# Performance work log

Hardware: AMD Instinct MI355X
Metric: run time of the kernel (lower is better)

The kernel has to match this reference:

```python
import jax, jax.numpy as jnp
import numpy as np

CUTOFF = 3.0   # self.cutoff
RMIN = 3.5     # rmin in cutoff_function (note rmin > cutoff, faithful to source)
ETA = 4.0
N_RADIAL = 5
N_3BODY = 12
NATOMS = 2048
K = 48         # neighbors per atom (equal counts -> ragged loop becomes dense batch)
HID = 64
NPAIRS = NATOMS * K


def setup_inputs() -> dict:
    key = jax.random.key(0)
    ks = jax.random.split(key, 4)
    # displacements scaled so |rij| is mostly within a few Angstrom
    rij = jax.random.normal(ks[0], (NPAIRS, 3), jnp.float32) * 1.5
    # sorted-by-atom pair list with K neighbors per atom
    unique_i = jnp.repeat(jnp.arange(NATOMS, dtype=jnp.int64), K)
    W1 = jax.random.normal(ks[1], (N_RADIAL + N_3BODY, HID), jnp.float32) * 0.1
    b1 = jnp.zeros((HID,), jnp.float32)
    W2 = jax.random.normal(ks[2], (HID, HID), jnp.float32) * 0.1
    b2 = jnp.zeros((HID,), jnp.float32)
    W3 = jax.random.normal(ks[3], (HID, 1), jnp.float32) * 0.1
    b3 = jnp.zeros((1,), jnp.float32)
    return dict(rij=rij, unique_i=unique_i, W1=W1, b1=b1, W2=W2, b2=b2, W3=W3, b3=b3)


def _energy(rij, W1, b1, W2, b2, W3, b3):
    d = jnp.linalg.norm(rij, axis=1, keepdims=True)           # (P,1)
    diff_norm = rij / jnp.maximum(d, 1e-12)                   # F.normalize
    # pair cutoff (rmin=3.5, c=3.0 as in source)
    fc = jnp.where(d > RMIN,
                   0.5 + 0.5 * jnp.cos(jnp.pi * (d - RMIN) / (CUTOFF - RMIN)),
                   1.0)
    # radial Bessel basis, n = 1..5
    ns = jnp.arange(1, N_RADIAL + 1, dtype=rij.dtype)
    rbf = jnp.sqrt(2.0 / CUTOFF) * jnp.sin(ns * jnp.pi / CUTOFF * d) / d * fc  # (P,5)
    # 3-body Gaussian descriptors
    fcrik = (0.5 + 0.5 * jnp.cos(jnp.pi * d / CUTOFF))[:, 0]  # (P,)
    dn = diff_norm.reshape(NATOMS, K, 3)
    cosang = jnp.einsum('nkd,nld->nkl', dn, dn)               # (N,K,K) pairwise mm
    cosang = jnp.where(jnp.eye(K, dtype=bool)[None], 0.0, cosang)  # fill_diagonal_(0)
    mu = jnp.linspace(-1.0, 1.0, N_3BODY).astype(rij.dtype)
    w = fcrik.reshape(NATOMS, 1, K, 1)                        # fcrik broadcast on axis being summed
    g3b = jnp.sum(jnp.exp(-ETA * (cosang[..., None] - mu) ** 2) * w, axis=2)  # (N,K,12)
    g3b = g3b.reshape(NPAIRS, N_3BODY)
    desc = jnp.concatenate([rbf, g3b], axis=1)                # (P,17)
    h = jnp.tanh(desc @ W1 + b1)
    h = jnp.tanh(h @ W2 + b2)
    eij = h @ W3 + b3                                         # (P,1)
    return jnp.sum(eij * fc)


def reference(rij, unique_i, W1, b1, W2, b2, W3, b3):
    # Module output: gradients of total energy w.r.t. rij (written into beta)
    return jax.grad(_energy)(rij, W1, b1, W2, b2, W3, b3)
```

## Files before the change

kernel.cpp:

```cpp
#include <hip/hip_runtime.h>
#include <hip/hip_bf16.h>

#define NATOMS 2048
#define K 48
#define P (NATOMS * K)
#define NR 5
#define NM 12
#define ND 17
#define HID 64

#define PI_F 3.14159265358979f
#define CUT 3.0f
#define RMIN_F 3.5f
#define AFC (-6.28318530717959f)
#define POC (PI_F / CUT)
#define SQ 0.816496580927726f
#define E1C 1.45454545454545f
#define CMC (-0.132231404958678f)

__device__ unsigned short g_desc[P * 32];
__device__ float g_gdesc[P * 20];
__device__ unsigned short g_w1t[64 * 32];
__device__ unsigned short g_w2t[64 * 64];
__device__ unsigned short g_w2r[64 * 64];
__device__ unsigned short g_w1r[32 * 64];

using frag_ab = __attribute__((ext_vector_type(8))) short;
using frag_cd = __attribute__((ext_vector_type(4))) float;

__device__ __forceinline__ float fast_tanh(float x) {
    float cx = fminf(fmaxf(x, -15.0f), 15.0f);
    float t = __expf(2.0f * cx);
    return (t - 1.0f) / (t + 1.0f);
}

__device__ __forceinline__ unsigned short f2bs(float x) {
    __hip_bfloat16 b = __float2bfloat16(x);
    return __builtin_bit_cast(unsigned short, b);
}

__global__ __launch_bounds__(256) void k_prep(const float* __restrict__ W1,
                                              const float* __restrict__ W2) {
    const int i = blockIdx.x * 256 + threadIdx.x;
    if (i < 2048) {
        const int n = i >> 5, k = i & 31;
        g_w1t[i] = (k < ND) ? f2bs(W1[k * HID + n]) : (unsigned short)0;
    } else if (i < 2048 + 4096) {
        const int j = i - 2048, n = j >> 6, k = j & 63;
        g_w2t[j] = f2bs(W2[k * HID + n]);
    } else if (i < 2048 + 8192) {
        const int j = i - (2048 + 4096);
        g_w2r[j] = f2bs(W2[j]);
    } else if (i < 2048 + 8192 + 2048) {
        const int j = i - (2048 + 8192), n = j >> 6;
        g_w1r[j] = (n < ND) ? f2bs(W1[j]) : (unsigned short)0;
    }
}

__global__ __launch_bounds__(192) void k_fwd_atom(const float* __restrict__ rij) {
    __shared__ float su[K][3];
    __shared__ float sfcrik[K];
    __shared__ float sc[K * (K + 1)];
    __shared__ float spart[4 * K * 13];
    __shared__ __align__(16) unsigned short sOut[K][32];
    const int atom = blockIdx.x, t = threadIdx.x, base = atom * K;

    if (t < K) {
        const float x = rij[3 * (base + t) + 0];
        const float y = rij[3 * (base + t) + 1];
        const float z = rij[3 * (base + t) + 2];
        const float d = sqrtf(x * x + y * y + z * z);
        const float inv = 1.0f / fmaxf(d, 1e-12f);
        su[t][0] = x * inv; su[t][1] = y * inv; su[t][2] = z * inv;
        sfcrik[t] = 0.5f + 0.5f * __cosf(POC * d);
        const float fc = (d > RMIN_F) ? (0.5f + 0.5f * __cosf(AFC * (d - RMIN_F))) : 1.0f;
        const float s = SQ * fc / d;
#pragma unroll
        for (int n = 0; n < NR; n++) {
            const float bn = (float)(n + 1) * POC;
            sOut[t][n] = f2bs(s * __sinf(bn * d));
        }
#pragma unroll
        for (int c = ND; c < 32; c++) sOut[t][c] = 0;
    }
    __syncthreads();

#pragma unroll
    for (int r = 0; r < 12; r++) {
        const int idx = t + r * 192;
        const int k = idx / K, l = idx - k * K;
        const float c = su[k][0] * su[l][0] + su[k][1] * su[l][1] + su[k][2] * su[l][2];
        sc[k * (K + 1) + l] = (k == l) ? 0.0f : c;
    }
    __syncthreads();

    {
        const int k = t % K, ch = t / K;
        float part[NM];
#pragma unroll
        for (int m = 0; m < NM; m++) part[m] = 0.0f;
#pragma unroll
        for (int li = 0; li < 12; li++) {
            const int l = ch * 12 + li;
            const float cp1 = sc[k * (K + 1) + l] + 1.0f;
            const float e0 = __expf(-4.0f * cp1 * cp1) * sfcrik[l];
            const float e1 = __expf(E1C * cp1);
            float tm = e0;
            part[0] += tm;
#pragma unroll
            for (int m = 1; m < NM; m++) { tm *= e1; part[m] += tm; }
        }
#pragma unroll
        for (int m = 0; m < NM; m++) spart[(ch * K + k) * 13 + m] = part[m];
    }
    __syncthreads();

#pragma unroll
    for (int r = 0; r < 3; r++) {
        const int idx = t + r * 192;
        const int k = idx / NM, m = idx - k * NM;
        const float cm = __expf(CMC * (float)(m * m));
        const float s = spart[(0 * K + k) * 13 + m] + spart[(1 * K + k) * 13 + m]
                      + spart[(2 * K + k) * 13 + m] + spart[(3 * K + k) * 13 + m];
        sOut[k][NR + m] = f2bs(s * cm);
    }
    __syncthreads();

    {
        const int r = t >> 2, c = (t & 3) * 8;
        *(uint4*)&g_desc[(base + r) * 32 + c] = *(const uint4*)&sOut[r][c];
    }
}

#define LW1 40
#define LW2 72
#define O_DESC 0
#define O_W1T  2560
#define O_W2T  5120
#define O_W2R  9728
#define O_W1R  14336
#define O_H1   16640
#define O_GZ2  21248
#define SM_SHORTS 25856

__global__ __launch_bounds__(256) void k_mlp(const float* __restrict__ rij,
                                             const float* __restrict__ b1,
                                             const float* __restrict__ b2,
                                             const float* __restrict__ W3,
                                             const float* __restrict__ b3) {
    __shared__ __align__(16) short sm[SM_SHORTS];
    __shared__ float sFc[64], sB1[64], sB2[64], sW3[64];

    const int t = threadIdx.x;
    const int base = blockIdx.x * 64;

    if (t < 64) {
        const int p = base + t;
        const float x = rij[3 * p], y = rij[3 * p + 1], z = rij[3 * p + 2];
        const float d = sqrtf(x * x + y * y + z * z);
        sFc[t] = (d > RMIN_F) ? (0.5f + 0.5f * __cosf(AFC * (d - RMIN_F))) : 1.0f;
        sB1[t] = b1[t]; sB2[t] = b2[t]; sW3[t] = W3[t];
    }
    {
        const int r = t >> 2, c = (t & 3) * 8;
        *(uint4*)&sm[O_DESC + r * LW1 + c] = *(const uint4*)&g_desc[(base + r) * 32 + c];
    }
    {
        const int n = t >> 2, c = (t & 3) * 8;
        *(uint4*)&sm[O_W1T + n * LW1 + c] = *(const uint4*)&g_w1t[n * 32 + c];
    }
#pragma unroll
    for (int rr = 0; rr < 2; rr++) {
        const int i = t + rr * 256, n = i >> 3, c = (i & 7) * 8;
        *(uint4*)&sm[O_W2T + n * LW2 + c] = *(const uint4*)&g_w2t[n * 64 + c];
    }
#pragma unroll
    for (int rr = 0; rr < 2; rr++) {
        const int i = t + rr * 256, n = i >> 3, c = (i & 7) * 8;
        *(uint4*)&sm[O_W2R + n * LW2 + c] = *(const uint4*)&g_w2r[n * 64 + c];
    }
    {
        const int n = t >> 3, c = (t & 7) * 8;
        *(uint4*)&sm[O_W1R + n * LW2 + c] = *(const uint4*)&g_w1r[n * 64 + c];
    }
    __syncthreads();

    const int w = t >> 6, lane = t & 63, quad = lane >> 4, lm = lane & 15;
    const int mrow = w * 16;

    float t1[16];
    {
        const frag_ab a = *(const frag_ab*)&sm[O_DESC + (mrow + lm) * LW1 + quad * 8];
#pragma unroll
        for (int nt = 0; nt < 4; nt++) {
            const frag_ab bf = *(const frag_ab*)&sm[O_W1T + (nt * 16 + lm) * LW1 + quad * 8];
            const float bias = sB1[nt * 16 + lm];
            frag_cd acc = {bias, bias, bias, bias};
            acc = __builtin_amdgcn_mfma_f32_16x16x32_bf16(a, bf, acc, 0, 0, 0);
#pragma unroll
            for (int r = 0; r < 4; r++) {
                const float tv = fast_tanh(acc[r]);
                t1[nt * 4 + r] = tv;
                sm[O_H1 + (mrow + quad * 4 + r) * LW2 + nt * 16 + lm] = (short)f2bs(tv);
            }
        }
    }

    float fcr[4];
#pragma unroll
    for (int r = 0; r < 4; r++) fcr[r] = sFc[mrow + quad * 4 + r];
    {
        const frag_ab a0 = *(const frag_ab*)&sm[O_H1 + (mrow + lm) * LW2 + quad * 8];
        const frag_ab a1 = *(const frag_ab*)&sm[O_H1 + (mrow + lm) * LW2 + 32 + quad * 8];
        float er[4] = {0.0f, 0.0f, 0.0f, 0.0f};
#pragma unroll
        for (int nt = 0; nt < 4; nt++) {
            const int n = nt * 16 + lm;
            const frag_ab b0 = *(const frag_ab*)&sm[O_W2T + n * LW2 + quad * 8];
            const frag_ab b1f = *(const frag_ab*)&sm[O_W2T + n * LW2 + 32 + quad * 8];
            const float bias = sB2[n];
            frag_cd acc = {bias, bias, bias, bias};
            acc = __builtin_amdgcn_mfma_f32_16x16x32_bf16(a0, b0, acc, 0, 0, 0);
            acc = __builtin_amdgcn_mfma_f32_16x16x32_bf16(a1, b1f, acc, 0, 0, 0);
            const float w3n = sW3[n];
#pragma unroll
            for (int r = 0; r < 4; r++) {
                const float tv = fast_tanh(acc[r]);
                er[r] = fmaf(tv, w3n, er[r]);
                sm[O_GZ2 + (mrow + quad * 4 + r) * LW2 + n] =
                    (short)f2bs(fcr[r] * w3n * (1.0f - tv * tv));
            }
        }
#pragma unroll
        for (int off = 1; off < 16; off <<= 1) {
#pragma unroll
            for (int r = 0; r < 4; r++) er[r] += __shfl_xor(er[r], off, 64);
        }
        if (lm == 0) {
            const float b3v = b3[0];
#pragma unroll
            for (int r = 0; r < 4; r++)
                g_gdesc[(base + mrow + quad * 4 + r) * 20 + 17] = er[r] + b3v;
        }
    }

    {
        const frag_ab a0 = *(const frag_ab*)&sm[O_GZ2 + (mrow + lm) * LW2 + quad * 8];
        const frag_ab a1 = *(const frag_ab*)&sm[O_GZ2 + (mrow + lm) * LW2 + 32 + quad * 8];
#pragma unroll
        for (int nt = 0; nt < 4; nt++) {
            const int n = nt * 16 + lm;
            const frag_ab b0 = *(const frag_ab*)&sm[O_W2R + n * LW2 + quad * 8];
            const frag_ab b1f = *(const frag_ab*)&sm[O_W2R + n * LW2 + 32 + quad * 8];
            frag_cd acc = {0.0f, 0.0f, 0.0f, 0.0f};
            acc = __builtin_amdgcn_mfma_f32_16x16x32_bf16(a0, b0, acc, 0, 0, 0);
            acc = __builtin_amdgcn_mfma_f32_16x16x32_bf16(a1, b1f, acc, 0, 0, 0);
#pragma unroll
            for (int r = 0; r < 4; r++) {
                const float g = acc[r] * (1.0f - t1[nt * 4 + r] * t1[nt * 4 + r]);
                sm[O_H1 + (mrow + quad * 4 + r) * LW2 + n] = (short)f2bs(g);
            }
        }
    }

    {
        const frag_ab a0 = *(const frag_ab*)&sm[O_H1 + (mrow + lm) * LW2 + quad * 8];
        const frag_ab a1 = *(const frag_ab*)&sm[O_H1 + (mrow + lm) * LW2 + 32 + quad * 8];
#pragma unroll
        for (int nt = 0; nt < 2; nt++) {
            const int n = nt * 16 + lm;
            const frag_ab b0 = *(const frag_ab*)&sm[O_W1R + n * LW2 + quad * 8];
            const frag_ab b1f = *(const frag_ab*)&sm[O_W1R + n * LW2 + 32 + quad * 8];
            frag_cd acc = {0.0f, 0.0f, 0.0f, 0.0f};
            acc = __builtin_amdgcn_mfma_f32_16x16x32_bf16(a0, b0, acc, 0, 0, 0);
            acc = __builtin_amdgcn_mfma_f32_16x16x32_bf16(a1, b1f, acc, 0, 0, 0);
            if (n < ND) {
#pragma unroll
                for (int r = 0; r < 4; r++)
                    g_gdesc[(base + mrow + quad * 4 + r) * 20 + n] = acc[r];
            }
        }
    }
}

__global__ __launch_bounds__(256) void k_bwd_atom(const float* __restrict__ rij,
                                                  float* __restrict__ out) {
    __shared__ float su[K][3];
    __shared__ float sd_[K];
    __shared__ float sfcrik[K];
    __shared__ float sS[K][K + 1];
    __shared__ float sT[K][K + 1];
    __shared__ float sgG[K][NM];
    __shared__ float sgu[K][3];
    __shared__ float sgf[K];
    const int atom = blockIdx.x, t = threadIdx.x, base = atom * K;

    if (t < K) {
        const float x = rij[3 * (base + t) + 0];
        const float y = rij[3 * (base + t) + 1];
        const float z = rij[3 * (base + t) + 2];
        const float d = sqrtf(x * x + y * y + z * z);
        const float inv = 1.0f / fmaxf(d, 1e-12f);
        su[t][0] = x * inv; su[t][1] = y * inv; su[t][2] = z * inv;
        sd_[t] = d;
        sfcrik[t] = 0.5f + 0.5f * __cosf(POC * d);
    }
    for (int idx = t; idx < K * NM; idx += 256) {
        const int k = idx / NM, m = idx - k * NM;
        sgG[k][m] = g_gdesc[(base + k) * 20 + NR + m] * __expf(CMC * (float)(m * m));
    }
    __syncthreads();

    for (int idx = t; idx < K * K; idx += 256) {
        const int k = idx / K, l = idx - k * K;
        const float c = su[k][0] * su[l][0] + su[k][1] * su[l][1] + su[k][2] * su[l][2];
        sS[k][l] = (k == l) ? 0.0f : c;
    }
    __syncthreads();

    for (int idx = t; idx < K * K; idx += 256) {
        const int k = idx / K, l = idx - k * K;
        const float cp1 = sS[k][l] + 1.0f;
        const float e0 = __expf(-4.0f * cp1 * cp1);
        const float e1 = __expf(E1C * cp1);
        float tm = e0;
        float T = sgG[k][0] * tm, U = 0.0f;
#pragma unroll
        for (int m = 1; m < NM; m++) {
            tm *= e1;
            const float q = sgG[k][m] * tm;
            T += q;
            U = fmaf((float)m, q, U);
        }
        const float Sp = cp1 * T - (2.0f / 11.0f) * U;
        sT[k][l] = T;
        sS[k][l] = (k == l) ? 0.0f : (-8.0f) * Sp;
    }
    __syncthreads();

    if (t < K) {
        float s = 0.0f;
#pragma unroll 4
        for (int kk = 0; kk < K; kk++) s += sT[kk][t];
        sgf[t] = s;
    } else if (t >= 64 && t < 64 + K) {
        const int k = t - 64;
        const float fk = sfcrik[k];
        float gx = 0.0f, gy = 0.0f, gz = 0.0f;
#pragma unroll 4
        for (int l = 0; l < K; l++) {
            const float w = fmaf(sS[k][l], sfcrik[l], sS[l][k] * fk);
            gx = fmaf(w, su[l][0], gx);
            gy = fmaf(w, su[l][1], gy);
            gz = fmaf(w, su[l][2], gz);
        }
        sgu[k][0] = gx; sgu[k][1] = gy; sgu[k][2] = gz;
    }
    __syncthreads();

    if (t < K) {
        const float d = sd_[t];
        const float ux = su[t][0], uy = su[t][1], uz = su[t][2];
        const float invd = 1.0f / d;
        float gfc = g_gdesc[(base + t) * 20 + 17];
        float gdR = 0.0f;
#pragma unroll
        for (int n = 0; n < NR; n++) {
            const float bn = (float)(n + 1) * POC;
            float sn, cn;
            __sincosf(bn * d, &sn, &cn);
            const float g = g_gdesc[(base + t) * 20 + n];
            gfc = fmaf(g, SQ * sn * invd, gfc);
            gdR = fmaf(g, SQ * (bn * cn - sn * invd) * invd, gdR);
        }
        float fc, dfc;
        if (d > RMIN_F) {
            float sa, ca;
            __sincosf(AFC * (d - RMIN_F), &sa, &ca);
            fc = 0.5f + 0.5f * ca;
            dfc = -0.5f * AFC * sa;
        } else { fc = 1.0f; dfc = 0.0f; }
        const float dfcrik = -0.5f * POC * __sinf(POC * d);

        const float gd = fc * gdR + gfc * dfc + sgf[t] * dfcrik;
        const float gux = sgu[t][0], guy = sgu[t][1], guz = sgu[t][2];
        const float dot = gux * ux + guy * uy + guz * uz;

        out[3 * (base + t) + 0] = fmaf(gd, ux, (gux - dot * ux) * invd);
        out[3 * (base + t) + 1] = fmaf(gd, uy, (guy - dot * uy) * invd);
        out[3 * (base + t) + 2] = fmaf(gd, uz, (guz - dot * uz) * invd);
    }
}

extern "C" void kernel_launch(void* const* d_in, const int* in_sizes, int n_in,
                              void* d_out, int out_size, void* d_ws, size_t ws_size,
                              hipStream_t stream) {
    (void)in_sizes; (void)n_in; (void)out_size; (void)d_ws; (void)ws_size;
    const float* rij = (const float*)d_in[0];
    const float* W1 = (const float*)d_in[2];
    const float* b1 = (const float*)d_in[3];
    const float* W2 = (const float*)d_in[4];
    const float* b2 = (const float*)d_in[5];
    const float* W3 = (const float*)d_in[6];
    const float* b3 = (const float*)d_in[7];
    float* out = (float*)d_out;

    k_prep<<<48, 256, 0, stream>>>(W1, W2);
    k_fwd_atom<<<NATOMS, 192, 0, stream>>>(rij);
    k_mlp<<<P / 64, 256, 0, stream>>>(rij, b1, b2, W3, b3);
    k_bwd_atom<<<NATOMS, 256, 0, stream>>>(rij, out);
}
```

Before: 111.8 us.

## Fuse forward descriptor, MLP and backward passes into one per-atom kernel

Merges the three kernels (forward descriptors, MLP forward/backward, per-atom backward) into a single kernel with one block per atom. Descriptors and descriptor gradients stay in shared memory instead of round-tripping through global buffers, and the cosine matrix is reused rather than recomputed. The MLP now works on 48 rows per block, with each wave owning one 16-column output slice and loading its weight fragments straight from global memory instead of staging them in LDS. The shared memory regions are aliased across phases to keep occupancy up, at the cost of extra barriers and less even MFMA work per wave.

Result: faster. 105.2 us (-5.9%).

```diff
diff --git a/kernel.cpp b/kernel.cpp
--- a/kernel.cpp
+++ b/kernel.cpp
@@ -18,8 +18,6 @@
 #define E1C 1.45454545454545f
 #define CMC (-0.132231404958678f)
 
-__device__ unsigned short g_desc[P * 32];
-__device__ float g_gdesc[P * 20];
 __device__ unsigned short g_w1t[64 * 32];
 __device__ unsigned short g_w2t[64 * 64];
 __device__ unsigned short g_w2r[64 * 64];
@@ -57,53 +55,92 @@
     }
 }
 
-__global__ __launch_bounds__(192) void k_fwd_atom(const float* __restrict__ rij) {
-    __shared__ float su[K][3];
-    __shared__ float sfcrik[K];
-    __shared__ float sc[K * (K + 1)];
-    __shared__ float spart[4 * K * 13];
-    __shared__ __align__(16) unsigned short sOut[K][32];
-    const int atom = blockIdx.x, t = threadIdx.x, base = atom * K;
+#define SC_OFF    0
+#define H1_OFF    9408
+#define GZ2_OFF   16320
+#define DESC_OFF  23232
+#define SPART_OFF 9408
+#define SGG_OFF   9408
+#define ST_OFF    16320
+#define SGD_OFF   27072
+#define SRIJ_OFF  30912
+#define SU_OFF    31488
+#define SFC_OFF   32064
+#define SFK_OFF   32256
+#define SD_OFF    32448
+#define SE_OFF    32640
+#define SGF_OFF   33408
+#define SGU_OFF   33600
+#define SM_BYTES  34176
+
+__global__ __launch_bounds__(256, 4) void k_fused(const float* __restrict__ rij,
+                                                  const float* __restrict__ b1,
+                                                  const float* __restrict__ b2,
+                                                  const float* __restrict__ W3,
+                                                  const float* __restrict__ b3,
+                                                  float* __restrict__ out) {
+    __shared__ __align__(16) char smem[SM_BYTES];
+    float* sc    = (float*)(smem + SC_OFF);
+    short* h1S   = (short*)(smem + H1_OFF);
+    short* gz2S  = (short*)(smem + GZ2_OFF);
+    short* descS = (short*)(smem + DESC_OFF);
+    float* spart = (float*)(smem + SPART_OFF);
+    float* sgG   = (float*)(smem + SGG_OFF);
+    float* sT    = (float*)(smem + ST_OFF);
+    float* sgd   = (float*)(smem + SGD_OFF);
+    float* srij  = (float*)(smem + SRIJ_OFF);
+    float* su    = (float*)(smem + SU_OFF);
+    float* sfc   = (float*)(smem + SFC_OFF);
+    float* sfk   = (float*)(smem + SFK_OFF);
+    float* sd    = (float*)(smem + SD_OFF);
+    float* se    = (float*)(smem + SE_OFF);
+    float* sgf   = (float*)(smem + SGF_OFF);
+    float* sgu   = (float*)(smem + SGU_OFF);
+
+    const int t = threadIdx.x;
+    const int base3 = blockIdx.x * (K * 3);
+
+    if (t < K * 3) srij[t] = rij[base3 + t];
+    __syncthreads();
 
     if (t < K) {
-        const float x = rij[3 * (base + t) + 0];
-        const float y = rij[3 * (base + t) + 1];
-        const float z = rij[3 * (base + t) + 2];
+        const float x = srij[3 * t], y = srij[3 * t + 1], z = srij[3 * t + 2];
         const float d = sqrtf(x * x + y * y + z * z);
         const float inv = 1.0f / fmaxf(d, 1e-12f);
-        su[t][0] = x * inv; su[t][1] = y * inv; su[t][2] = z * inv;
-        sfcrik[t] = 0.5f + 0.5f * __cosf(POC * d);
+        su[3 * t] = x * inv; su[3 * t + 1] = y * inv; su[3 * t + 2] = z * inv;
+        sd[t] = d;
+        sfk[t] = 0.5f + 0.5f * __cosf(POC * d);
         const float fc = (d > RMIN_F) ? (0.5f + 0.5f * __cosf(AFC * (d - RMIN_F))) : 1.0f;
+        sfc[t] = fc;
         const float s = SQ * fc / d;
 #pragma unroll
         for (int n = 0; n < NR; n++) {
             const float bn = (float)(n + 1) * POC;
-            sOut[t][n] = f2bs(s * __sinf(bn * d));
-        }
-#pragma unroll
-        for (int c = ND; c < 32; c++) sOut[t][c] = 0;
-    }
-    __syncthreads();
-
-#pragma unroll
-    for (int r = 0; r < 12; r++) {
-        const int idx = t + r * 192;
+            descS[t * 40 + n] = (short)f2bs(s * __sinf(bn * d));
+        }
+#pragma unroll
+        for (int c = ND; c < 32; c++) descS[t * 40 + c] = 0;
+    }
+    __syncthreads();
+
+    for (int idx = t; idx < K * K; idx += 256) {
         const int k = idx / K, l = idx - k * K;
-        const float c = su[k][0] * su[l][0] + su[k][1] * su[l][1] + su[k][2] * su[l][2];
-        sc[k * (K + 1) + l] = (k == l) ? 0.0f : c;
-    }
-    __syncthreads();
-
-    {
-        const int k = t % K, ch = t / K;
+        const float c = su[3 * k] * su[3 * l] + su[3 * k + 1] * su[3 * l + 1]
+                      + su[3 * k + 2] * su[3 * l + 2];
+        sc[k * 49 + l] = (k == l) ? 0.0f : c;
+    }
+    __syncthreads();
+
+    if (t < 192) {
+        const int ch = t / 48, k = t - ch * 48;
         float part[NM];
 #pragma unroll
         for (int m = 0; m < NM; m++) part[m] = 0.0f;
 #pragma unroll
         for (int li = 0; li < 12; li++) {
             const int l = ch * 12 + li;
-            const float cp1 = sc[k * (K + 1) + l] + 1.0f;
-            const float e0 = __expf(-4.0f * cp1 * cp1) * sfcrik[l];
+            const float cp1 = sc[k * 49 + l] + 1.0f;
+            const float e0 = __expf(-4.0f * cp1 * cp1) * sfk[l];
             const float e1 = __expf(E1C * cp1);
             float tm = e0;
             part[0] += tm;
@@ -111,284 +148,185 @@
             for (int m = 1; m < NM; m++) { tm *= e1; part[m] += tm; }
         }
 #pragma unroll
-        for (int m = 0; m < NM; m++) spart[(ch * K + k) * 13 + m] = part[m];
-    }
-    __syncthreads();
-
-#pragma unroll
-    for (int r = 0; r < 3; r++) {
-        const int idx = t + r * 192;
+        for (int m = 0; m < NM; m++) spart[(ch * 48 + k) * 13 + m] = part[m];
+    }
+    __syncthreads();
+
+    for (int idx = t; idx < K * NM; idx += 256) {
         const int k = idx / NM, m = idx - k * NM;
         const float cm = __expf(CMC * (float)(m * m));
-        const float s = spart[(0 * K + k) * 13 + m] + spart[(1 * K + k) * 13 + m]
-                      + spart[(2 * K + k) * 13 + m] + spart[(3 * K + k) * 13 + m];
-        sOut[k][NR + m] = f2bs(s * cm);
-    }
-    __syncthreads();
-
+        const float s = spart[(0 * 48 + k) * 13 + m] + spart[(1 * 48 + k) * 13 + m]
+                      + spart[(2 * 48 + k) * 13 + m] + spart[(3 * 48 + k) * 13 + m];
+        descS[k * 40 + NR + m] = (short)f2bs(s * cm);
+    }
+    __syncthreads();
+
+    const int w = t >> 6, lane = t & 63, quad = lane >> 4, lm = lane & 15;
+    const int n0 = w * 16 + lm;
+
+    float t1[3][4];
     {
-        const int r = t >> 2, c = (t & 3) * 8;
-        *(uint4*)&g_desc[(base + r) * 32 + c] = *(const uint4*)&sOut[r][c];
-    }
-}
-
-#define LW1 40
-#define LW2 72
-#define O_DESC 0
-#define O_W1T  2560
-#define O_W2T  5120
-#define O_W2R  9728
-#define O_W1R  14336
-#define O_H1   16640
-#define O_GZ2  21248
-#define SM_SHORTS 25856
-
-__global__ __launch_bounds__(256) void k_mlp(const float* __restrict__ rij,
-                                             const float* __restrict__ b1,
-                                             const float* __restrict__ b2,
-                                             const float* __restrict__ W3,
-                                             const float* __restrict__ b3) {
-    __shared__ __align__(16) short sm[SM_SHORTS];
-    __shared__ float sFc[64], sB1[64], sB2[64], sW3[64];
-
-    const int t = threadIdx.x;
-    const int base = blockIdx.x * 64;
-
-    if (t < 64) {
-        const int p = base + t;
-        const float x = rij[3 * p], y = rij[3 * p + 1], z = rij[3 * p + 2];
-        const float d = sqrtf(x * x + y * y + z * z);
-        sFc[t] = (d > RMIN_F) ? (0.5f + 0.5f * __cosf(AFC * (d - RMIN_F))) : 1.0f;
-        sB1[t] = b1[t]; sB2[t] = b2[t]; sW3[t] = W3[t];
-    }
-    {
-        const int r = t >> 2, c = (t & 3) * 8;
-        *(uint4*)&sm[O_DESC + r * LW1 + c] = *(const uint4*)&g_desc[(base + r) * 32 + c];
-    }
-    {
-        const int n = t >> 2, c = (t & 3) * 8;
-        *(uint4*)&sm[O_W1T + n * LW1 + c] = *(const uint4*)&g_w1t[n * 32 + c];
-    }
-#pragma unroll
-    for (int rr = 0; rr < 2; rr++) {
-        const int i = t + rr * 256, n = i >> 3, c = (i & 7) * 8;
-        *(uint4*)&sm[O_W2T + n * LW2 + c] = *(const uint4*)&g_w2t[n * 64 + c];
-    }
-#pragma unroll
-    for (int rr = 0; rr < 2; rr++) {
-        const int i = t + rr * 256, n = i >> 3, c = (i & 7) * 8;
-        *(uint4*)&sm[O_W2R + n * LW2 + c] = *(const uint4*)&g_w2r[n * 64 + c];
-    }
-    {
-        const int n = t >> 3, c = (t & 7) * 8;
-        *(uint4*)&sm[O_W1R + n * LW2 + c] = *(const uint4*)&g_w1r[n * 64 + c];
-    }
-    __syncthreads();
-
-    const int w = t >> 6, lane = t & 63, quad = lane >> 4, lm = lane & 15;
-    const int mrow = w * 16;
-
-    float t1[16];
-    {
-        const frag_ab a = *(const frag_ab*)&sm[O_DESC + (mrow + lm) * LW1 + quad * 8];
-#pragma unroll
-        for (int nt = 0; nt < 4; nt++) {
-            const frag_ab bf = *(const frag_ab*)&sm[O_W1T + (nt * 16 + lm) * LW1 + quad * 8];
-            const float bias = sB1[nt * 16 + lm];
+        const frag_ab bf = *(const frag_ab*)&g_w1t[n0 * 32 + quad * 8];
+        const float bias = b1[n0];
+#pragma unroll
+        for (int mt = 0; mt < 3; mt++) {
+            const frag_ab a = *(const frag_ab*)&descS[(mt * 16 + lm) * 40 + quad * 8];
             frag_cd acc = {bias, bias, bias, bias};
             acc = __builtin_amdgcn_mfma_f32_16x16x32_bf16(a, bf, acc, 0, 0, 0);
 #pragma unroll
             for (int r = 0; r < 4; r++) {
                 const float tv = fast_tanh(acc[r]);
-                t1[nt * 4 + r] = tv;
-                sm[O_H1 + (mrow + quad * 4 + r) * LW2 + nt * 16 + lm] = (short)f2bs(tv);
-            }
-        }
-    }
-
-    float fcr[4];
-#pragma unroll
-    for (int r = 0; r < 4; r++) fcr[r] = sFc[mrow + quad * 4 + r];
+                t1[mt][r] = tv;
+                h1S[(mt * 16 + quad * 4 + r) * 72 + n0] = (short)f2bs(tv);
+            }
+        }
+    }
+    __syncthreads();
+
     {
-        const frag_ab a0 = *(const frag_ab*)&sm[O_H1 + (mrow + lm) * LW2 + quad * 8];
-        const frag_ab a1 = *(const frag_ab*)&sm[O_H1 + (mrow + lm) * LW2 + 32 + quad * 8];
-        float er[4] = {0.0f, 0.0f, 0.0f, 0.0f};
-#pragma unroll
-        for (int nt = 0; nt < 4; nt++) {
-            const int n = nt * 16 + lm;
-            const frag_ab b0 = *(const frag_ab*)&sm[O_W2T + n * LW2 + quad * 8];
-            const frag_ab b1f = *(const frag_ab*)&sm[O_W2T + n * LW2 + 32 + quad * 8];
-            const float bias = sB2[n];
+        const frag_ab b0 = *(const frag_ab*)&g_w2t[n0 * 64 + quad * 8];
+        const frag_ab b1f = *(const frag_ab*)&g_w2t[n0 * 64 + 32 + quad * 8];
+        const float bias = b2[n0];
+        const float w3n = W3[n0];
+#pragma unroll
+        for (int mt = 0; mt < 3; mt++) {
+            const frag_ab a0 = *(const frag_ab*)&h1S[(mt * 16 + lm) * 72 + quad * 8];
+            const frag_ab a1 = *(const frag_ab*)&h1S[(mt * 16 + lm) * 72 + 32 + quad * 8];
             frag_cd acc = {bias, bias, bias, bias};
             acc = __builtin_amdgcn_mfma_f32_16x16x32_bf16(a0, b0, acc, 0, 0, 0);
             acc = __builtin_amdgcn_mfma_f32_16x16x32_bf16(a1, b1f, acc, 0, 0, 0);
-            const float w3n = sW3[n];
+            float ep[4];
 #pragma unroll
             for (int r = 0; r < 4; r++) {
+                const int row = mt * 16 + quad * 4 + r;
                 const float tv = fast_tanh(acc[r]);
-                er[r] = fmaf(tv, w3n, er[r]);
-                sm[O_GZ2 + (mrow + quad * 4 + r) * LW2 + n] =
-                    (short)f2bs(fcr[r] * w3n * (1.0f - tv * tv));
-            }
-        }
-#pragma unroll
-        for (int off = 1; off < 16; off <<= 1) {
-#pragma unroll
-            for (int r = 0; r < 4; r++) er[r] += __shfl_xor(er[r], off, 64);
-        }
-        if (lm == 0) {
-            const float b3v = b3[0];
-#pragma unroll
-            for (int r = 0; r < 4; r++)
-                g_gdesc[(base + mrow + quad * 4 + r) * 20 + 17] = er[r] + b3v;
-        }
-    }
+                ep[r] = tv * w3n;
+                gz2S[row * 72 + n0] = (short)f2bs(sfc[row] * w3n * (1.0f - tv * tv));
+            }
+#pragma unroll
+            for (int off = 1; off < 16; off <<= 1) {
+#pragma unroll
+                for (int r = 0; r < 4; r++) ep[r] += __shfl_xor(ep[r], off, 64);
+            }
+            if (lm == 0) {
+#pragma unroll
+                for (int r = 0; r < 4; r++) se[w * 48 + mt * 16 + quad * 4 + r] = ep[r];
+            }
+        }
+    }
+    __syncthreads();
 
     {
-        const frag_ab a0 = *(const frag_ab*)&sm[O_GZ2 + (mrow + lm) * LW2 + quad * 8];
-        const frag_ab a1 = *(const frag_ab*)&sm[O_GZ2 + (mrow + lm) * LW2 + 32 + quad * 8];
-#pragma unroll
-        for (int nt = 0; nt < 4; nt++) {
-            const int n = nt * 16 + lm;
-            const frag_ab b0 = *(const frag_ab*)&sm[O_W2R + n * LW2 + quad * 8];
-            const frag_ab b1f = *(const frag_ab*)&sm[O_W2R + n * LW2 + 32 + quad * 8];
+        const frag_ab b0 = *(const frag_ab*)&g_w2r[n0 * 64 + quad * 8];
+        const frag_ab b1f = *(const frag_ab*)&g_w2r[n0 * 64 + 32 + quad * 8];
+#pragma unroll
+        for (int mt = 0; mt < 3; mt++) {
+            const frag_ab a0 = *(const frag_ab*)&gz2S[(mt * 16 + lm) * 72 + quad * 8];
+            const frag_ab a1 = *(const frag_ab*)&gz2S[(mt * 16 + lm) * 72 + 32 + quad * 8];
             frag_cd acc = {0.0f, 0.0f, 0.0f, 0.0f};
             acc = __builtin_amdgcn_mfma_f32_16x16x32_bf16(a0, b0, acc, 0, 0, 0);
             acc = __builtin_amdgcn_mfma_f32_16x16x32_bf16(a1, b1f, acc, 0, 0, 0);
 #pragma unroll
             for (int r = 0; r < 4; r++) {
-                const float g = acc[r] * (1.0f - t1[nt * 4 + r] * t1[nt * 4 + r]);
-                sm[O_H1 + (mrow + quad * 4 + r) * LW2 + n] = (short)f2bs(g);
-            }
-        }
-    }
-
-    {
-        const frag_ab a0 = *(const frag_ab*)&sm[O_H1 + (mrow + lm) * LW2 + quad * 8];
-        const frag_ab a1 = *(const frag_ab*)&sm[O_H1 + (mrow + lm) * LW2 + 32 + quad * 8];
-#pragma unroll
-        for (int nt = 0; nt < 2; nt++) {
-            const int n = nt * 16 + lm;
-            const frag_ab b0 = *(const frag_ab*)&sm[O_W1R + n * LW2 + quad * 8];
-            const frag_ab b1f = *(const frag_ab*)&sm[O_W1R + n * LW2 + 32 + quad * 8];
-            frag_cd acc = {0.0f, 0.0f, 0.0f, 0.0f};
-            acc = __builtin_amdgcn_mfma_f32_16x16x32_bf16(a0, b0, acc, 0, 0, 0);
-            acc = __builtin_amdgcn_mfma_f32_16x16x32_bf16(a1, b1f, acc, 0, 0, 0);
-            if (n < ND) {
-#pragma unroll
-                for (int r = 0; r < 4; r++)
-                    g_gdesc[(base + mrow + quad * 4 + r) * 20 + n] = acc[r];
-            }
-        }
-    }
-}
-
-__global__ __launch_bounds__(256) void k_bwd_atom(const float* __restrict__ rij,
-                                                  float* __restrict__ out) {
-    __shared__ float su[K][3];
-    __shared__ float sd_[K];
-    __shared__ float sfcrik[K];
-    __shared__ float sS[K][K + 1];
-    __shared__ float sT[K][K + 1];
-    __shared__ float sgG[K][NM];
-    __shared__ float sgu[K][3];
-    __shared__ float sgf[K];
-    const int atom = blockIdx.x, t = threadIdx.x, base = atom * K;
-
-    if (t < K) {
-        const float x = rij[3 * (base + t) + 0];
-        const float y = rij[3 * (base + t) + 1];
-        const float z = rij[3 * (base + t) + 2];
-        const float d = sqrtf(x * x + y * y + z * z);
-        const float inv = 1.0f / fmaxf(d, 1e-12f);
-        su[t][0] = x * inv; su[t][1] = y * inv; su[t][2] = z * inv;
-        sd_[t] = d;
-        sfcrik[t] = 0.5f + 0.5f * __cosf(POC * d);
-    }
+                const float g = acc[r] * (1.0f - t1[mt][r] * t1[mt][r]);
+                h1S[(mt * 16 + quad * 4 + r) * 72 + n0] = (short)f2bs(g);
+            }
+        }
+    }
+    __syncthreads();
+
+    for (int tid = w; tid < 6; tid += 4) {
+        const int mt = tid >> 1, nt = tid & 1, n = nt * 16 + lm;
+        const frag_ab b0 = *(const frag_ab*)&g_w1r[n * 64 + quad * 8];
+        const frag_ab b1f = *(const frag_ab*)&g_w1r[n * 64 + 32 + quad * 8];
+        const frag_ab a0 = *(const frag_ab*)&h1S[(mt * 16 + lm) * 72 + quad * 8];
+        const frag_ab a1 = *(const frag_ab*)&h1S[(mt * 16 + lm) * 72 + 32 + quad * 8];
+        frag_cd acc = {0.0f, 0.0f, 0.0f, 0.0f};
+        acc = __builtin_amdgcn_mfma_f32_16x16x32_bf16(a0, b0, acc, 0, 0, 0);
+        acc = __builtin_amdgcn_mfma_f32_16x16x32_bf16(a1, b1f, acc, 0, 0, 0);
+        if (n < ND) {
+#pragma unroll
+            for (int r = 0; r < 4; r++)
+                sgd[(mt * 16 + quad * 4 + r) * 20 + n] = acc[r];
+        }
+    }
+    if (t < K)
+        sgd[t * 20 + 17] = se[t] + se[48 + t] + se[96 + t] + se[144 + t] + b3[0];
+    __syncthreads();
+
     for (int idx = t; idx < K * NM; idx += 256) {
         const int k = idx / NM, m = idx - k * NM;
-        sgG[k][m] = g_gdesc[(base + k) * 20 + NR + m] * __expf(CMC * (float)(m * m));
+        sgG[idx] = sgd[k * 20 + NR + m] * __expf(CMC * (float)(m * m));
     }
     __syncthreads();
 
     for (int idx = t; idx < K * K; idx += 256) {
         const int k = idx / K, l = idx - k * K;
-        const float c = su[k][0] * su[l][0] + su[k][1] * su[l][1] + su[k][2] * su[l][2];
-        sS[k][l] = (k == l) ? 0.0f : c;
-    }
-    __syncthreads();
-
-    for (int idx = t; idx < K * K; idx += 256) {
-        const int k = idx / K, l = idx - k * K;
-        const float cp1 = sS[k][l] + 1.0f;
+        const float cp1 = sc[k * 49 + l] + 1.0f;
         const float e0 = __expf(-4.0f * cp1 * cp1);
         const float e1 = __expf(E1C * cp1);
         float tm = e0;
-        float T = sgG[k][0] * tm, U = 0.0f;
+        float T = sgG[k * 12] * tm, U = 0.0f;
 #pragma unroll
         for (int m = 1; m < NM; m++) {
             tm *= e1;
-            const float q = sgG[k][m] * tm;
+            const float q = sgG[k * 12 + m] * tm;
             T += q;
             U = fmaf((float)m, q, U);
         }
         const float Sp = cp1 * T - (2.0f / 11.0f) * U;
-        sT[k][l] = T;
-        sS[k][l] = (k == l) ? 0.0f : (-8.0f) * Sp;
+        sT[k * 48 + l] = T;
+        sc[k * 49 + l] = (k == l) ? 0.0f : (-8.0f) * Sp;
     }
     __syncthreads();
 
     if (t < K) {
         float s = 0.0f;
 #pragma unroll 4
-        for (int kk = 0; kk < K; kk++) s += sT[kk][t];
+        for (int kk = 0; kk < K; kk++) s += sT[kk * 48 + t];
         sgf[t] = s;
     } else if (t >= 64 && t < 64 + K) {
         const int k = t - 64;
-        const float fk = sfcrik[k];
+        const float fk = sfk[k];
         float gx = 0.0f, gy = 0.0f, gz = 0.0f;
 #pragma unroll 4
         for (int l = 0; l < K; l++) {
-            const float w = fmaf(sS[k][l], sfcrik[l], sS[l][k] * fk);
-            gx = fmaf(w, su[l][0], gx);
-            gy = fmaf(w, su[l][1], gy);
-            gz = fmaf(w, su[l][2], gz);
-        }
-        sgu[k][0] = gx; sgu[k][1] = gy; sgu[k][2] = gz;
+            const float wgt = fmaf(sc[k * 49 + l], sfk[l], sc[l * 49 + k] * fk);
+            gx = fmaf(wgt, su[3 * l], gx);
+            gy = fmaf(wgt, su[3 * l + 1], gy);
+            gz = fmaf(wgt, su[3 * l + 2], gz);
+        }
+        sgu[3 * k] = gx; sgu[3 * k + 1] = gy; sgu[3 * k + 2] = gz;
     }
     __syncthreads();
 
     if (t < K) {
-        const float d = sd_[t];
-        const float ux = su[t][0], uy = su[t][1], uz = su[t][2];
+        const float d = sd[t];
+        const float ux = su[3 * t], uy = su[3 * t + 1], uz = su[3 * t + 2];
         const float invd = 1.0f / d;
-        float gfc = g_gdesc[(base + t) * 20 + 17];
+        float gfc = sgd[t * 20 + 17];
         float gdR = 0.0f;
 #pragma unroll
         for (int n = 0; n < NR; n++) {
             const float bn = (float)(n + 1) * POC;
             float sn, cn;
             __sincosf(bn * d, &sn, &cn);
-            const float g = g_gdesc[(base + t) * 20 + n];
+            const float g = sgd[t * 20 + n];
             gfc = fmaf(g, SQ * sn * invd, gfc);
             gdR = fmaf(g, SQ * (bn * cn - sn * invd) * invd, gdR);
         }
-        float fc, dfc;
-        if (d > RMIN_F) {
-            float sa, ca;
-            __sincosf(AFC * (d - RMIN_F), &sa, &ca);
-            fc = 0.5f + 0.5f * ca;
-            dfc = -0.5f * AFC * sa;
-        } else { fc = 1.0f; dfc = 0.0f; }
+        const float fc = sfc[t];
+        float dfc = 0.0f;
+        if (d > RMIN_F) dfc = -0.5f * AFC * __sinf(AFC * (d - RMIN_F));
         const float dfcrik = -0.5f * POC * __sinf(POC * d);
 
         const float gd = fc * gdR + gfc * dfc + sgf[t] * dfcrik;
-        const float gux = sgu[t][0], guy = sgu[t][1], guz = sgu[t][2];
+        const float gux = sgu[3 * t], guy = sgu[3 * t + 1], guz = sgu[3 * t + 2];
         const float dot = gux * ux + guy * uy + guz * uz;
 
-        out[3 * (base + t) + 0] = fmaf(gd, ux, (gux - dot * ux) * invd);
-        out[3 * (base + t) + 1] = fmaf(gd, uy, (guy - dot * uy) * invd);
-        out[3 * (base + t) + 2] = fmaf(gd, uz, (guz - dot * uz) * invd);
+        out[base3 + 3 * t + 0] = fmaf(gd, ux, (gux - dot * ux) * invd);
+        out[base3 + 3 * t + 1] = fmaf(gd, uy, (guy - dot * uy) * invd);
+        out[base3 + 3 * t + 2] = fmaf(gd, uz, (guz - dot * uz) * invd);
     }
 }
 
@@ -406,7 +344,5 @@
     float* out = (float*)d_out;
 
     k_prep<<<48, 256, 0, stream>>>(W1, W2);
-    k_fwd_atom<<<NATOMS, 192, 0, stream>>>(rij);
-    k_mlp<<<P / 64, 256, 0, stream>>>(rij, b1, b2, W3, b3);
-    k_bwd_atom<<<NATOMS, 256, 0, stream>>>(rij, out);
-}
+    k_fused<<<NATOMS, 256, 0, stream>>>(rij, b1, b2, W3, b3, out);
+}
```
